# Performance work log

Measured on AMD Instinct MI355X. Metric: run time of the kernel, lower is better.

## Reference

```python
import jax, jax.numpy as jnp
import numpy as np

EMBED_DIM = 1024
NUM_HEADS = 16
HEAD_DIM = EMBED_DIM // NUM_HEADS
SEQ = 2048
BSZ = 2


def setup_inputs() -> dict:
    key = jax.random.key(0)
    ks = jax.random.split(key, 12)
    f = jnp.float32
    query = jax.random.normal(ks[0], (SEQ, BSZ, EMBED_DIM), f)
    k_in = jax.random.normal(ks[1], (SEQ, BSZ, EMBED_DIM), f)
    v_in = jax.random.normal(ks[2], (SEQ, BSZ, EMBED_DIM), f)
    s = 0.02  # weight init scale
    q_w = jax.random.normal(ks[3], (EMBED_DIM, EMBED_DIM), f) * s
    q_b = jax.random.normal(ks[4], (EMBED_DIM,), f) * s
    k_w = jax.random.normal(ks[5], (EMBED_DIM, EMBED_DIM), f) * s
    k_b = jax.random.normal(ks[6], (EMBED_DIM,), f) * s
    v_w = jax.random.normal(ks[7], (EMBED_DIM, EMBED_DIM), f) * s
    v_b = jax.random.normal(ks[8], (EMBED_DIM,), f) * s
    o_w_mean = jax.random.normal(ks[9], (EMBED_DIM, EMBED_DIM), f) * s
    # lgstd ~ uniform(2*log(stdv), log(stdv)) with stdv = 1/sqrt(out+1)
    stdv = 1.0 / np.sqrt(EMBED_DIM + 1)
    o_w_lgstd = jax.random.uniform(ks[10], (EMBED_DIM, EMBED_DIM), f,
                                   2.0 * np.log(stdv), np.log(stdv))
    eps = jax.random.normal(ks[11], (EMBED_DIM, EMBED_DIM), f) * 1.5  # N(0, 1.5)
    return dict(query=query, key=k_in, value=v_in,
                q_w=q_w, q_b=q_b, k_w=k_w, k_b=k_b, v_w=v_w, v_b=v_b,
                o_w_mean=o_w_mean, o_w_lgstd=o_w_lgstd, eps=eps)


def reference(query, key, value, q_w, q_b, k_w, k_b, v_w, v_b,
              o_w_mean, o_w_lgstd, eps):
    tgt_len, bsz, embed_dim = query.shape
    scaling = HEAD_DIM ** -0.5
    # projections (F.linear: x @ W.T + b)
    q = (query @ q_w.T + q_b) * scaling          # [S,B,E]
    k = key @ k_w.T + k_b                        # [S,B,E]
    v = value @ v_w.T + v_b                      # [S,B,E]
    # [S,B,E] -> [B*H, S, hd]
    def split_heads(x, L):
        return x.reshape(L, bsz * NUM_HEADS, HEAD_DIM).transpose(1, 0, 2)
    q = split_heads(q, tgt_len)
    k = split_heads(k, key.shape[0])
    v = split_heads(v, value.shape[0])
    src_len = k.shape[1]
    scores = jnp.einsum('bqd,bkd->bqk', q, k)    # [B*H, S, S] (explicit O(n^2))
    attn = jax.nn.softmax(scores, axis=-1)
    ctx = jnp.einsum('bqk,bkd->bqd', attn, v)    # [B*H, S, hd]
    ctx = ctx.transpose(1, 0, 2).reshape(tgt_len, bsz, embed_dim)
    # Bayesian output projection: sampled weight (training mode), no bias
    o_w = o_w_mean + eps * jnp.exp(o_w_lgstd)
    out = ctx @ o_w.T                            # [S,B,E]
    avg_attn = attn.reshape(bsz, NUM_HEADS, tgt_len, src_len).sum(axis=1) / NUM_HEADS
    return out, avg_attn
```

## Files before the change

kernel.cpp:

```cpp
#include <hip/hip_runtime.h>

#define SQ 2048
#define BB 2
#define EE 1024
#define HH 16
#define DD 64
#define MM (SQ*BB)
#define NSLICE 4
#define KSLICE (SQ/NSLICE)
#define KT_IN (KSLICE/128)
#define LOG2E 1.44269504f

typedef _Float16 f16;
typedef _Float16 half8 __attribute__((ext_vector_type(8)));
typedef _Float16 half4 __attribute__((ext_vector_type(4)));
typedef float f32x4 __attribute__((ext_vector_type(4)));

static __device__ __forceinline__ f32x4 mfma16(half8 a, half8 b, f32x4 c) {
    return __builtin_amdgcn_mfma_f32_16x16x32_f16(a, b, c, 0, 0, 0);
}

static __device__ __forceinline__ void gload16(const f16* g, f16* l) {
    __builtin_amdgcn_global_load_lds(
        (const __attribute__((address_space(1))) unsigned int*)g,
        (__attribute__((address_space(3))) unsigned int*)l, 16, 0, 0);
}

__global__ void k_elem(const float* __restrict__ q_w, const float* __restrict__ k_w,
                       const float* __restrict__ v_w, const float* __restrict__ query,
                       const float* __restrict__ key, const float* __restrict__ value,
                       const float* __restrict__ owm, const float* __restrict__ owl,
                       const float* __restrict__ eps,
                       f16* qw16, f16* kw16, f16* vw16,
                       f16* xq16, f16* xk16, f16* xv16, f16* ow16)
{
    int y = blockIdx.y;
    size_t i = ((size_t)blockIdx.x * 256 + threadIdx.x) * 4;
    if (y < 3) {
        if (i >= (size_t)EE*EE) return;
        const float* s = (y==0) ? q_w : (y==1) ? k_w : v_w;
        f16* d = (y==0) ? qw16 : (y==1) ? kw16 : vw16;
        float4 v = *(const float4*)&s[i];
        half4 o = {(f16)v.x, (f16)v.y, (f16)v.z, (f16)v.w};
        *(half4*)&d[i] = o;
    } else if (y < 6) {
        const float* s = (y==3) ? query : (y==4) ? key : value;
        f16* d = (y==3) ? xq16 : (y==4) ? xk16 : xv16;
        float4 v = *(const float4*)&s[i];
        half4 o = {(f16)v.x, (f16)v.y, (f16)v.z, (f16)v.w};
        *(half4*)&d[i] = o;
    } else {
        if (i >= (size_t)EE*EE) return;
        float4 m = *(const float4*)&owm[i];
        float4 l = *(const float4*)&owl[i];
        float4 e = *(const float4*)&eps[i];
        half4 o = {(f16)(m.x + e.x * __expf(l.x)), (f16)(m.y + e.y * __expf(l.y)),
                   (f16)(m.z + e.z * __expf(l.z)), (f16)(m.w + e.w * __expf(l.w))};
        *(half4*)&ow16[i] = o;
    }
}

__device__ __forceinline__ void gemm_body(
    const f16* __restrict__ A, const f16* __restrict__ W,
    const float* __restrict__ bias, float scale, void* __restrict__ out, int mode)
{
    __shared__ f16 As[128*32];
    __shared__ f16 Bs[64*32];
    int t = threadIdx.x, lane = t & 63, w = t >> 6;
    int quad = lane >> 4, m16 = lane & 15;
    int wm = w >> 1, wn = w & 1;
    int gm0 = blockIdx.x * 128, gn0 = blockIdx.y * 64;
    int arow = lane >> 2, apch = lane & 3;
    f32x4 acc[4][2] = {};
    for (int kt = 0; kt < EE; kt += 32) {
        #pragma unroll
        for (int j = 0; j < 2; ++j) {
            int row = w*32 + j*16 + arow;
            int lch = apch ^ (row & 3);
            gload16(&A[(size_t)(gm0+row)*EE + kt + lch*8], &As[row*32 + apch*8]);
        }
        {
            int row = w*16 + arow;
            int lch = apch ^ (row & 3);
            gload16(&W[(size_t)(gn0+row)*EE + kt + lch*8], &Bs[row*32 + apch*8]);
        }
        __syncthreads();
        int cs = (quad ^ (m16 & 3)) * 8;
        half8 af[4], bf[2];
        #pragma unroll
        for (int i = 0; i < 4; ++i) af[i] = *(half8*)&As[(wm*64 + i*16 + m16)*32 + cs];
        #pragma unroll
        for (int j = 0; j < 2; ++j) bf[j] = *(half8*)&Bs[(wn*32 + j*16 + m16)*32 + cs];
        #pragma unroll
        for (int i = 0; i < 4; ++i)
            #pragma unroll
            for (int j = 0; j < 2; ++j)
                acc[i][j] = mfma16(af[i], bf[j], acc[i][j]);
        __syncthreads();
    }
    #pragma unroll
    for (int j = 0; j < 2; ++j) {
        int col = gn0 + wn*32 + j*16 + m16;
        float bb = bias ? bias[col] : 0.0f;
        #pragma unroll
        for (int i = 0; i < 4; ++i) {
            int r0 = gm0 + wm*64 + i*16 + quad*4;
            #pragma unroll
            for (int r = 0; r < 4; ++r) {
                float v = (acc[i][j][r] + bb) * scale;
                int m = r0 + r;
                if (mode == 2)      ((float*)out)[(size_t)m*EE + col] = v;
                else if (mode == 1) ((f16*)out)[((size_t)(m & 1)*EE + col)*SQ + (m >> 1)] = (f16)v;
                else                ((f16*)out)[(size_t)m*EE + col] = (f16)v;
            }
        }
    }
}

__global__ __launch_bounds__(256) void k_gemm_qkv(
    const f16* xq, const f16* qw, const float* qb,
    const f16* xk, const f16* kw, const float* kb,
    const f16* xv, const f16* vw, const float* vb,
    f16* Q16, f16* K16, f16* Vt16)
{
    int z = blockIdx.z;
    const f16* A = (z==0) ? xq : (z==1) ? xk : xv;
    const f16* W = (z==0) ? qw : (z==1) ? kw : vw;
    const float* bi = (z==0) ? qb : (z==1) ? kb : vb;
    float sc = (z==0) ? 0.125f * LOG2E : 1.0f;
    void* o = (z==0) ? (void*)Q16 : (z==1) ? (void*)K16 : (void*)Vt16;
    gemm_body(A, W, bi, sc, o, (z==2) ? 1 : 0);
}

__global__ __launch_bounds__(256) void k_gemm_o(const f16* A, const f16* W, float* out)
{
    gemm_body(A, W, nullptr, 1.0f, out, 2);
}

__global__ __launch_bounds__(256, 4) void k_attn_l(
    const f16* __restrict__ Q16, const f16* __restrict__ K16, float* __restrict__ lse2)
{
    __shared__ float red[4][64];
    const int t = threadIdx.x, lane = t & 63, w = t >> 6;
    const int quad = lane >> 4, m16 = lane & 15;
    const int q0 = blockIdx.x * 64, h = blockIdx.y, b = blockIdx.z;

    half8 bq[4][2];
    #pragma unroll
    for (int nt = 0; nt < 4; ++nt)
        #pragma unroll
        for (int dk = 0; dk < 2; ++dk)
            bq[nt][dk] = *(const half8*)&Q16[(size_t)((q0 + nt*16 + m16)*BB + b)*EE + h*DD + dk*32 + quad*8];

    float lsum[4] = {};
    for (int kt = 0; kt < 16; ++kt) {
        half8 ak[2][2];
        #pragma unroll
        for (int mt = 0; mt < 2; ++mt)
            #pragma unroll
            for (int dk = 0; dk < 2; ++dk)
                ak[mt][dk] = *(const half8*)&K16[(size_t)((kt*128 + w*32 + mt*16 + m16)*BB + b)*EE + h*DD + dk*32 + quad*8];
        #pragma unroll
        for (int mt = 0; mt < 2; ++mt)
            #pragma unroll
            for (int nt = 0; nt < 4; ++nt) {
                f32x4 s = {};
                s = mfma16(ak[mt][0], bq[nt][0], s);
                s = mfma16(ak[mt][1], bq[nt][1], s);
                lsum[nt] += __builtin_amdgcn_exp2f(s[0]) + __builtin_amdgcn_exp2f(s[1])
                          + __builtin_amdgcn_exp2f(s[2]) + __builtin_amdgcn_exp2f(s[3]);
            }
    }
    #pragma unroll
    for (int nt = 0; nt < 4; ++nt) {
        float v = lsum[nt];
        v += __shfl_xor(v, 16, 64);
        v += __shfl_xor(v, 32, 64);
        lsum[nt] = v;
    }
    if (quad == 0)
        #pragma unroll
        for (int nt = 0; nt < 4; ++nt) red[w][nt*16 + m16] = lsum[nt];
    __syncthreads();
    if (t < 64) {
        float v = red[0][t] + red[1][t] + red[2][t] + red[3][t];
        lse2[((size_t)b*HH + h)*SQ + q0 + t] = __log2f(v);
    }
}

__global__ __launch_bounds__(256, 2) void k_attn_main(
    const f16* __restrict__ Q16, const f16* __restrict__ K16, const f16* __restrict__ Vt16,
    const float* __restrict__ lse2, float* __restrict__ ctxp, float* __restrict__ avg_out)
{
    __shared__ f16 ps[2][32][136];
    __shared__ float csh[HH][32];
    const int t = threadIdx.x, lane = t & 63, w = t >> 6;
    const int quad = lane >> 4, m16 = lane & 15;
    const int q0 = blockIdx.x * 32, sl = blockIdx.y, b = blockIdx.z;
    const int ks0 = sl * KSLICE;

    for (int i = t; i < HH*32; i += 256) {
        int hh = i >> 5, qq = i & 31;
        csh[hh][qq] = lse2[((size_t)b*HH + hh)*SQ + q0 + qq];
    }
    __syncthreads();

    float avg_r[KT_IN][16] = {};

    for (int hp = 0; hp < 8; ++hp) {
        f32x4 acc[2][2] = {};
        for (int hh2 = 0; hh2 < 2; ++hh2) {
            const int h = hp*2 + hh2;
            half8 bq[2][2];
            #pragma unroll
            for (int nt = 0; nt < 2; ++nt)
                #pragma unroll
                for (int dk = 0; dk < 2; ++dk)
                    bq[nt][dk] = *(const half8*)&Q16[(size_t)((q0 + nt*16 + m16)*BB + b)*EE + h*DD + dk*32 + quad*8];
            const float c01[2] = { csh[h][m16], csh[h][16 + m16] };

            half8 ak[2][2][2], bv[2][4];
            #pragma unroll
            for (int mt = 0; mt < 2; ++mt)
                #pragma unroll
                for (int dk = 0; dk < 2; ++dk)
                    ak[0][mt][dk] = *(const half8*)&K16[(size_t)((ks0 + w*32 + mt*16 + m16)*BB + b)*EE + h*DD + dk*32 + quad*8];
            #pragma unroll
            for (int ks = 0; ks < 4; ++ks)
                bv[0][ks] = *(const half8*)&Vt16[((size_t)b*EE + h*DD + w*16 + m16)*SQ + ks0 + ks*32 + quad*8];

            #pragma unroll
            for (int kt = 0; kt < KT_IN; ++kt) {
                const int cur = kt & 1, nxt = cur ^ 1;
                if (kt + 1 < KT_IN) {
                    #pragma unroll
                    for (int mt = 0; mt < 2; ++mt)
                        #pragma unroll
                        for (int dk = 0; dk < 2; ++dk)
                            ak[nxt][mt][dk] = *(const half8*)&K16[(size_t)((ks0 + (kt+1)*128 + w*32 + mt*16 + m16)*BB + b)*EE + h*DD + dk*32 + quad*8];
                    #pragma unroll
                    for (int ks = 0; ks < 4; ++ks)
                        bv[nxt][ks] = *(const half8*)&Vt16[((size_t)b*EE + h*DD + w*16 + m16)*SQ + ks0 + (kt+1)*128 + ks*32 + quad*8];
                }
                #pragma unroll
                for (int mt = 0; mt < 2; ++mt)
                    #pragma unroll
                    for (int nt = 0; nt < 2; ++nt) {
                        f32x4 s = {};
                        s = mfma16(ak[cur][mt][0], bq[nt][0], s);
                        s = mfma16(ak[cur][mt][1], bq[nt][1], s);
                        half4 ph;
                        #pragma unroll
                        for (int r = 0; r < 4; ++r) {
                            float p = __builtin_amdgcn_exp2f(s[r] - c01[nt]);
                            avg_r[kt][mt*8 + nt*4 + r] += p;
                            ph[r] = (f16)p;
                        }
                        *(half4*)&ps[cur][nt*16 + m16][w*32 + mt*16 + quad*4] = ph;
                    }
                __builtin_amdgcn_sched_barrier(0);
                __builtin_amdgcn_s_waitcnt(0xC07F);
                __builtin_amdgcn_s_barrier();
                __builtin_amdgcn_sched_barrier(0);
                #pragma unroll
                for (int qt = 0; qt < 2; ++qt) {
                    f32x4 c4 = acc[hh2][qt];
                    #pragma unroll
                    for (int ks = 0; ks < 4; ++ks) {
                        half8 ap = *(half8*)&ps[cur][qt*16 + m16][ks*32 + quad*8];
                        c4 = mfma16(ap, bv[cur][ks], c4);
                    }
                    acc[hh2][qt] = c4;
                }
            }
        }
        #pragma unroll
        for (int hh2 = 0; hh2 < 2; ++hh2)
            #pragma unroll
            for (int qt = 0; qt < 2; ++qt)
                #pragma unroll
                for (int r = 0; r < 4; ++r) {
                    int q = q0 + qt*16 + quad*4 + r;
                    ctxp[(size_t)sl*MM*EE + ((size_t)q*BB + b)*EE + (hp*2 + hh2)*DD + w*16 + m16] = acc[hh2][qt][r];
                }
    }
    #pragma unroll
    for (int kt = 0; kt < KT_IN; ++kt)
        #pragma unroll
        for (int mt = 0; mt < 2; ++mt)
            #pragma unroll
            for (int nt = 0; nt < 2; ++nt) {
                int q = q0 + nt*16 + m16;
                int k = ks0 + kt*128 + w*32 + mt*16 + quad*4;
                float4 v = { avg_r[kt][mt*8+nt*4+0]*(1.0f/HH), avg_r[kt][mt*8+nt*4+1]*(1.0f/HH),
                             avg_r[kt][mt*8+nt*4+2]*(1.0f/HH), avg_r[kt][mt*8+nt*4+3]*(1.0f/HH) };
                *(float4*)&avg_out[((size_t)b*SQ + q)*SQ + k] = v;
            }
}

__global__ void k_ctx_red(const float* __restrict__ ctxp, f16* __restrict__ ctx16) {
    size_t i = ((size_t)blockIdx.x * 256 + threadIdx.x) * 4;
    float4 s = *(const float4*)&ctxp[i];
    #pragma unroll
    for (int sl = 1; sl < NSLICE; ++sl) {
        float4 v = *(const float4*)&ctxp[(size_t)sl*MM*EE + i];
        s.x += v.x; s.y += v.y; s.z += v.z; s.w += v.w;
    }
    half4 o = {(f16)s.x, (f16)s.y, (f16)s.z, (f16)s.w};
    *(half4*)&ctx16[i] = o;
}

extern "C" void kernel_launch(void* const* d_in, const int* in_sizes, int n_in,
                              void* d_out, int out_size, void* d_ws, size_t ws_size,
                              hipStream_t stream) {
    const float* query    = (const float*)d_in[0];
    const float* key      = (const float*)d_in[1];
    const float* value    = (const float*)d_in[2];
    const float* q_w      = (const float*)d_in[3];
    const float* q_b      = (const float*)d_in[4];
    const float* k_w      = (const float*)d_in[5];
    const float* k_b      = (const float*)d_in[6];
    const float* v_w      = (const float*)d_in[7];
    const float* v_b      = (const float*)d_in[8];
    const float* o_w_mean = (const float*)d_in[9];
    const float* o_w_lgstd= (const float*)d_in[10];
    const float* eps      = (const float*)d_in[11];
    float* out = (float*)d_out;
    float* avg = out + (size_t)MM * EE;

    const size_t EWN = (size_t)EE*EE;
    const size_t XWN = (size_t)MM*EE;
    f16* qw16  = (f16*)d_ws;
    f16* kw16  = qw16 + EWN;
    f16* vw16  = kw16 + EWN;
    f16* ow16  = vw16 + EWN;
    f16* Q16   = ow16 + EWN;
    f16* K16   = Q16  + XWN;
    f16* Vt16  = K16  + XWN;
    f16* ctx16 = Vt16 + XWN;
    float* lse2 = (float*)(ctx16 + XWN);
    f16* xq16  = (f16*)(lse2 + (size_t)BB*HH*SQ);
    f16* xk16  = xq16 + XWN;
    f16* xv16  = xk16 + XWN;
    float* ctxp = (float*)xq16;

    k_elem<<<dim3(XWN/1024, 7), 256, 0, stream>>>(q_w, k_w, v_w, query, key, value,
        o_w_mean, o_w_lgstd, eps, qw16, kw16, vw16, xq16, xk16, xv16, ow16);

    k_gemm_qkv<<<dim3(MM/128, EE/64, 3), 256, 0, stream>>>(
        xq16, qw16, q_b, xk16, kw16, k_b, xv16, vw16, v_b, Q16, K16, Vt16);

    k_attn_l   <<<dim3(SQ/64, HH, BB), 256, 0, stream>>>(Q16, K16, lse2);
    k_attn_main<<<dim3(SQ/32, NSLICE, BB), 256, 0, stream>>>(Q16, K16, Vt16, lse2, ctxp, avg);
    k_ctx_red  <<<XWN/1024, 256, 0, stream>>>(ctxp, ctx16);

    k_gemm_o<<<dim3(MM/128, EE/64), 256, 0, stream>>>(ctx16, ow16, out);
}
```

Baseline: 394.8 us.

## Store Q/K/V projections in head-major contiguous layout for attention loads

The QKV GEMM epilogue now writes Q and K as [B,H,S,D] and V as [B,H,S/32,D,32] tiles instead of the interleaved [S,B,E] and [B,E,S] layouts. The attention kernels index per-head base pointers, so each K/Q/V fragment load touches a contiguous head block and has better cache-line and TLB locality. The cost is more scattered stores in the GEMM epilogue, especially for the tiled V layout.

```diff
diff --git a/kernel.cpp b/kernel.cpp
--- a/kernel.cpp
+++ b/kernel.cpp
@@ -101,6 +101,7 @@
     #pragma unroll
     for (int j = 0; j < 2; ++j) {
         int col = gn0 + wn*32 + j*16 + m16;
+        int h = col >> 6, d = col & 63;
         float bb = bias ? bias[col] : 0.0f;
         #pragma unroll
         for (int i = 0; i < 4; ++i) {
@@ -109,9 +110,13 @@
             for (int r = 0; r < 4; ++r) {
                 float v = (acc[i][j][r] + bb) * scale;
                 int m = r0 + r;
-                if (mode == 2)      ((float*)out)[(size_t)m*EE + col] = v;
-                else if (mode == 1) ((f16*)out)[((size_t)(m & 1)*EE + col)*SQ + (m >> 1)] = (f16)v;
-                else                ((f16*)out)[(size_t)m*EE + col] = (f16)v;
+                int s = m >> 1, b = m & 1;
+                if (mode == 2)
+                    ((float*)out)[(size_t)m*EE + col] = v;
+                else if (mode == 1)
+                    ((f16*)out)[((((size_t)b*HH + h)*(SQ/32) + (s >> 5))*DD + d)*32 + (s & 31)] = (f16)v;
+                else
+                    ((f16*)out)[(((size_t)b*HH + h)*SQ + s)*DD + d] = (f16)v;
             }
         }
     }
@@ -144,13 +149,15 @@
     const int t = threadIdx.x, lane = t & 63, w = t >> 6;
     const int quad = lane >> 4, m16 = lane & 15;
     const int q0 = blockIdx.x * 64, h = blockIdx.y, b = blockIdx.z;
+    const f16* Qh = Q16 + ((size_t)b*HH + h)*SQ*DD;
+    const f16* Kh = K16 + ((size_t)b*HH + h)*SQ*DD;
 
     half8 bq[4][2];
     #pragma unroll
     for (int nt = 0; nt < 4; ++nt)
         #pragma unroll
         for (int dk = 0; dk < 2; ++dk)
-            bq[nt][dk] = *(const half8*)&Q16[(size_t)((q0 + nt*16 + m16)*BB + b)*EE + h*DD + dk*32 + quad*8];
+            bq[nt][dk] = *(const half8*)&Qh[(q0 + nt*16 + m16)*DD + dk*32 + quad*8];
 
     float lsum[4] = {};
     for (int kt = 0; kt < 16; ++kt) {
@@ -159,7 +166,7 @@
         for (int mt = 0; mt < 2; ++mt)
             #pragma unroll
             for (int dk = 0; dk < 2; ++dk)
-                ak[mt][dk] = *(const half8*)&K16[(size_t)((kt*128 + w*32 + mt*16 + m16)*BB + b)*EE + h*DD + dk*32 + quad*8];
+                ak[mt][dk] = *(const half8*)&Kh[(kt*128 + w*32 + mt*16 + m16)*DD + dk*32 + quad*8];
         #pragma unroll
         for (int mt = 0; mt < 2; ++mt)
             #pragma unroll
@@ -211,12 +218,15 @@
         f32x4 acc[2][2] = {};
         for (int hh2 = 0; hh2 < 2; ++hh2) {
             const int h = hp*2 + hh2;
+            const f16* Qh = Q16 + ((size_t)b*HH + h)*SQ*DD;
+            const f16* Kh = K16 + ((size_t)b*HH + h)*SQ*DD;
+            const f16* Vh = Vt16 + ((size_t)b*HH + h)*(SQ/32)*DD*32;
             half8 bq[2][2];
             #pragma unroll
             for (int nt = 0; nt < 2; ++nt)
                 #pragma unroll
                 for (int dk = 0; dk < 2; ++dk)
-                    bq[nt][dk] = *(const half8*)&Q16[(size_t)((q0 + nt*16 + m16)*BB + b)*EE + h*DD + dk*32 + quad*8];
+                    bq[nt][dk] = *(const half8*)&Qh[(q0 + nt*16 + m16)*DD + dk*32 + quad*8];
             const float c01[2] = { csh[h][m16], csh[h][16 + m16] };
 
             half8 ak[2][2][2], bv[2][4];
@@ -224,10 +234,10 @@
             for (int mt = 0; mt < 2; ++mt)
                 #pragma unroll
                 for (int dk = 0; dk < 2; ++dk)
-                    ak[0][mt][dk] = *(const half8*)&K16[(size_t)((ks0 + w*32 + mt*16 + m16)*BB + b)*EE + h*DD + dk*32 + quad*8];
+                    ak[0][mt][dk] = *(const half8*)&Kh[(ks0 + w*32 + mt*16 + m16)*DD + dk*32 + quad*8];
             #pragma unroll
             for (int ks = 0; ks < 4; ++ks)
-                bv[0][ks] = *(const half8*)&Vt16[((size_t)b*EE + h*DD + w*16 + m16)*SQ + ks0 + ks*32 + quad*8];
+                bv[0][ks] = *(const half8*)&Vh[(((ks0 + ks*32) >> 5)*DD + w*16 + m16)*32 + quad*8];
 
             #pragma unroll
             for (int kt = 0; kt < KT_IN; ++kt) {
@@ -237,10 +247,10 @@
                     for (int mt = 0; mt < 2; ++mt)
                         #pragma unroll
                         for (int dk = 0; dk < 2; ++dk)
-                            ak[nxt][mt][dk] = *(const half8*)&K16[(size_t)((ks0 + (kt+1)*128 + w*32 + mt*16 + m16)*BB + b)*EE + h*DD + dk*32 + quad*8];
+                            ak[nxt][mt][dk] = *(const half8*)&Kh[(ks0 + (kt+1)*128 + w*32 + mt*16 + m16)*DD + dk*32 + quad*8];
                     #pragma unroll
                     for (int ks = 0; ks < 4; ++ks)
-                        bv[nxt][ks] = *(const half8*)&Vt16[((size_t)b*EE + h*DD + w*16 + m16)*SQ + ks0 + (kt+1)*128 + ks*32 + quad*8];
+                        bv[nxt][ks] = *(const half8*)&Vh[(((ks0 + (kt+1)*128 + ks*32) >> 5)*DD + w*16 + m16)*32 + quad*8];
                 }
                 #pragma unroll
                 for (int mt = 0; mt < 2; ++mt)
```

Result: faster. 371.5 us (-5.9%).
